# Kernel tuning notes

Measured on AMD Instinct MI355X. Metric: run time of the kernel, lower is better.

## Reference

```python
import jax, jax.numpy as jnp
import numpy as np
import math

B, S, D = 1, 2048, 2048
NH, NKV = 32, 8
HD = D // NH  # 64
N_REP = NH // NKV


def _rope_tables(seq_len, head_dim, base=10000.0):
    half = head_dim // 2
    inv_freq = 1.0 / (base ** (np.arange(half, dtype=np.float32) / half))
    ang = np.arange(seq_len, dtype=np.float32)[:, None] * inv_freq[None, :]  # [S, half]
    ang = np.concatenate([ang, ang], axis=-1)  # [S, head_dim]
    cos = jnp.asarray(np.cos(ang))[:, None, :]  # [S, 1, head_dim]
    sin = jnp.asarray(np.sin(ang))[:, None, :]
    return cos, sin


def setup_inputs() -> dict:
    key = jax.random.key(0)
    ks = jax.random.split(key, 5)
    x = jax.random.normal(ks[0], (B, S, D), dtype=jnp.float32)
    cos, sin = _rope_tables(S, HD)
    # causal additive mask, broadcast over batch/heads
    neg = jnp.float32(-1e9)
    causal = jnp.where(jnp.tril(jnp.ones((S, S), dtype=bool)), 0.0, neg)
    mask = causal[None, None, :, :]  # [1,1,S,S]
    scale = 0.02
    wq = jax.random.normal(ks[1], (D, NH * HD), dtype=jnp.float32) * scale
    wk = jax.random.normal(ks[2], (D, NKV * HD), dtype=jnp.float32) * scale
    wv = jax.random.normal(ks[3], (D, NKV * HD), dtype=jnp.float32) * scale
    wo = jax.random.normal(ks[4], (NH * HD, D), dtype=jnp.float32) * scale
    return {"x": x, "cos": cos, "sin": sin, "mask": mask,
            "wq": wq, "wk": wk, "wv": wv, "wo": wo}


def apply_rotary_emb(x, cos, sin):
    # x: [b, s, h, d]; cos/sin: [s, 1, d] (broadcast over b, h)
    half = x.shape[-1] // 2
    x1, x2 = x[..., :half], x[..., half:]
    c, s = cos[..., :half], sin[..., :half]
    return jnp.concatenate([x1 * c - x2 * s, x1 * s + x2 * c], axis=-1)


def reference(x, cos, sin, mask, wq, wk, wv, wo):
    b, s, _ = x.shape
    q = (x @ wq).reshape(b, s, NH, HD)
    k = (x @ wk).reshape(b, s, NKV, HD)
    v = (x @ wv).reshape(b, s, NKV, HD)
    q = apply_rotary_emb(q, cos, sin)
    k = apply_rotary_emb(k, cos, sin)
    new_k, new_v = k, v  # kv cache (no previous cache)
    # GQA: repeat_interleave kv heads to match query heads
    k_rep = jnp.repeat(k, N_REP, axis=2)  # [b, s, NH, HD]
    v_rep = jnp.repeat(v, N_REP, axis=2)
    scores = jnp.einsum('bqhd,bkhd->bhqk', q, k_rep) / math.sqrt(HD)
    scores = scores + mask[:, :, -s:, :]
    attn = jax.nn.softmax(scores.astype(jnp.float32), axis=-1).astype(q.dtype)
    out = jnp.einsum('bhqk,bkhd->bqhd', attn, v_rep).reshape(b, s, NH * HD)
    return out @ wo, new_k, new_v
```

## Files before the change

### kernel.cpp

```cpp
#include <hip/hip_runtime.h>

#define S_LEN 2048
#define NHQ 32
#define NKV 8
#define HD 64
#define DMODEL 2048
#define DKV 512

typedef unsigned short ushort_t;
typedef unsigned int uint_t;

typedef __attribute__((ext_vector_type(8))) short bf16x8;
typedef __attribute__((ext_vector_type(4))) float f32x4;

__device__ __forceinline__ float b2f(ushort_t h) {
  union { uint_t u; float f; } v;
  v.u = ((uint_t)h) << 16;
  return v.f;
}
__device__ __forceinline__ ushort_t f2b(float f) {
  union { float f; uint_t u; } v;
  v.f = f;
  uint_t r = v.u + 0x7fffu + ((v.u >> 16) & 1u);
  return (ushort_t)(r >> 16);
}
__device__ __forceinline__ uint_t cvt_pk_bf16(float lo, float hi) {
  uint_t r;
  asm("v_cvt_pk_bf16_f32 %0, %1, %2" : "=v"(r) : "v"(lo), "v"(hi));
  return r;
}

union BF8 { uint4 v; ushort_t s[8]; };

__device__ __forceinline__ void gl_lds16(const ushort_t* g, ushort_t* l) {
  __builtin_amdgcn_global_load_lds((const __attribute__((address_space(1))) void*)g,
                                   (__attribute__((address_space(3))) void*)l, 16, 0, 0);
}

__device__ __forceinline__ void wT_tile(const float* __restrict__ W,
                                        ushort_t* __restrict__ WT,
                                        int K, int N, int r0, int c0,
                                        ushort_t (*T)[66], int tid) {
  {
    const int rl = tid >> 2, cp = (tid & 3) * 16;
    const float* p = W + (size_t)(r0 + rl) * N + c0 + cp;
    float v[16];
    *(float4*)(v)      = *(const float4*)(p);
    *(float4*)(v + 4)  = *(const float4*)(p + 4);
    *(float4*)(v + 8)  = *(const float4*)(p + 8);
    *(float4*)(v + 12) = *(const float4*)(p + 12);
    #pragma unroll
    for (int j = 0; j < 16; ++j) T[cp + j][rl] = f2b(v[j]);
  }
  __syncthreads();
  {
    const int cl = tid >> 2, rp = (tid & 3) * 16;
    uint_t u[8];
    #pragma unroll
    for (int i = 0; i < 8; ++i) u[i] = *(const uint_t*)&T[cl][rp + 2 * i];
    ushort_t* outp = WT + (size_t)(c0 + cl) * K + r0 + rp;
    *(uint4*)(outp)     = make_uint4(u[0], u[1], u[2], u[3]);
    *(uint4*)(outp + 8) = make_uint4(u[4], u[5], u[6], u[7]);
  }
}

__global__ __launch_bounds__(256) void prework(const float* __restrict__ X,
                                               ushort_t* __restrict__ XB,
                                               const float* __restrict__ Wq,
                                               const float* __restrict__ Wk,
                                               const float* __restrict__ Wv,
                                               ushort_t* __restrict__ WqT,
                                               ushort_t* __restrict__ WkvT) {
  __shared__ ushort_t T[64][66];
  const int tid = threadIdx.x;
  const int bid = blockIdx.x;
  if (bid < 2048) {
    int i = (bid * 256 + tid) * 8;
    float4 a = *(const float4*)(X + i);
    float4 b = *(const float4*)(X + i + 4);
    BF8 u;
    u.s[0] = f2b(a.x); u.s[1] = f2b(a.y); u.s[2] = f2b(a.z); u.s[3] = f2b(a.w);
    u.s[4] = f2b(b.x); u.s[5] = f2b(b.y); u.s[6] = f2b(b.z); u.s[7] = f2b(b.w);
    *(uint4*)(XB + i) = u.v;
    return;
  }
  const float* W; ushort_t* WT; int N; int local;
  if (bid < 3072)      { local = bid - 2048; W = Wq; WT = WqT;  N = DMODEL; }
  else if (bid < 3328) { local = bid - 3072; W = Wk; WT = WkvT; N = DKV; }
  else                 { local = bid - 3328; W = Wv; WT = WkvT + (size_t)DKV * DMODEL; N = DKV; }
  const int r0 = (local & 31) * 64, c0 = (local >> 5) * 64;
  wT_tile(W, WT, DMODEL, N, r0, c0, T, tid);
}

__global__ __launch_bounds__(256) void postproj(const float* __restrict__ Wo,
                                                ushort_t* __restrict__ WoT,
                                                float* Kio, ushort_t* __restrict__ KB,
                                                const float* __restrict__ cosT,
                                                const float* __restrict__ sinT,
                                                const float* __restrict__ V,
                                                ushort_t* __restrict__ VT) {
  __shared__ ushort_t T[64][66];
  const int tid = threadIdx.x;
  const int bid = blockIdx.x;
  if (bid < 1024) {
    const int r0 = (bid & 31) * 64, c0 = (bid >> 5) * 64;
    wT_tile(Wo, WoT, DMODEL, DMODEL, r0, c0, T, tid);
    return;
  }
  if (bid < 3072) {
    int idx = (bid - 1024) * 256 + tid;
    int d = idx & 31;
    int hk = (idx >> 5) & 7;
    int s = idx >> 8;
    float* p = Kio + (size_t)s * DKV + hk * HD + d;
    float x1 = p[0], x2 = p[32];
    float c = cosT[s * 64 + d], sn = sinT[s * 64 + d];
    float n1 = x1 * c - x2 * sn;
    float n2 = x1 * sn + x2 * c;
    p[0] = n1; p[32] = n2;
    ushort_t* kb = KB + (size_t)hk * S_LEN * HD + (size_t)s * HD + d;
    kb[0] = f2b(n1); kb[32] = f2b(n2);
    return;
  }
  {
    const int local = bid - 3072;
    const int s0 = (local & 31) * 64;
    const int hk = local >> 5;
    {
      const int s_l = tid >> 2, dp = (tid & 3) * 16;
      const float* p = V + (size_t)(s0 + s_l) * DKV + hk * HD + dp;
      float v[16];
      *(float4*)(v)      = *(const float4*)(p);
      *(float4*)(v + 4)  = *(const float4*)(p + 4);
      *(float4*)(v + 8)  = *(const float4*)(p + 8);
      *(float4*)(v + 12) = *(const float4*)(p + 12);
      #pragma unroll
      for (int j = 0; j < 16; ++j) T[dp + j][s_l] = f2b(v[j]);
    }
    __syncthreads();
    {
      const int d_l = tid >> 2, sp = (tid & 3) * 16;
      uint_t u[8];
      #pragma unroll
      for (int i = 0; i < 8; ++i) u[i] = *(const uint_t*)&T[d_l][sp + 2 * i];
      ushort_t* outp = VT + (size_t)hk * HD * S_LEN + (size_t)d_l * S_LEN + s0 + sp;
      *(uint4*)(outp)     = make_uint4(u[0], u[1], u[2], u[3]);
      *(uint4*)(outp + 8) = make_uint4(u[4], u[5], u[6], u[7]);
    }
  }
}

__device__ __forceinline__ void gemm_core_db64(const ushort_t* __restrict__ A,
                                               const ushort_t* __restrict__ BT,
                                               int K, int tile_m, int tile_n,
                                               f32x4 (&acc)[4][2],
                                               ushort_t* AsBase,
                                               ushort_t* BsBase) {
  const int tid = threadIdx.x;
  const int lane = tid & 63;
  const int w = tid >> 6;
  const int wr = (w >> 2) * 64, wc = (w & 3) * 32;
  const int lm = lane & 15, kq = lane >> 4;
  const int BUF = 2 * 128 * 32;
  const int HALF = 128 * 32;

  #pragma unroll
  for (int i = 0; i < 4; ++i)
    #pragma unroll
    for (int j = 0; j < 2; ++j) acc[i][j] = {0.f, 0.f, 0.f, 0.f};

  const ushort_t* ap = A  + (size_t)(tile_m + w * 16 + (lane >> 2)) * K + (lane & 3) * 8;
  const ushort_t* bp = BT + (size_t)(tile_n + w * 16 + (lane >> 2)) * K + (lane & 3) * 8;
  ushort_t* asw = AsBase + w * 512;
  ushort_t* bsw = BsBase + w * 512;

  gl_lds16(ap,      asw);
  gl_lds16(ap + 32, asw + HALF);
  gl_lds16(bp,      bsw);
  gl_lds16(bp + 32, bsw + HALF);
  __syncthreads();

  int cur = 0;
  for (int kt = 0; kt < K; kt += 64) {
    if (kt + 64 < K) {
      const int nb = (cur ^ 1) * BUF;
      gl_lds16(ap + kt + 64, asw + nb);
      gl_lds16(ap + kt + 96, asw + nb + HALF);
      gl_lds16(bp + kt + 64, bsw + nb);
      gl_lds16(bp + kt + 96, bsw + nb + HALF);
    }
    const ushort_t* ac = AsBase + cur * BUF;
    const ushort_t* bc = BsBase + cur * BUF;
    #pragma unroll
    for (int kc = 0; kc < 2; ++kc) {
      bf16x8 af[4], bfr[2];
      #pragma unroll
      for (int i = 0; i < 4; ++i)
        af[i]  = *(const bf16x8*)(ac + kc * HALF + (wr + 16 * i + lm) * 32 + kq * 8);
      #pragma unroll
      for (int j = 0; j < 2; ++j)
        bfr[j] = *(const bf16x8*)(bc + kc * HALF + (wc + 16 * j + lm) * 32 + kq * 8);
      #pragma unroll
      for (int i = 0; i < 4; ++i)
        #pragma unroll
        for (int j = 0; j < 2; ++j)
          acc[i][j] = __builtin_amdgcn_mfma_f32_16x16x32_bf16(af[i], bfr[j], acc[i][j], 0, 0, 0);
    }
    __syncthreads();
    cur ^= 1;
  }
}

__global__ __launch_bounds__(512) void gemm_proj(const ushort_t* __restrict__ A,
                                                 const ushort_t* __restrict__ BT,
                                                 ushort_t* __restrict__ Qo,
                                                 float* __restrict__ Ko,
                                                 float* __restrict__ Vo) {
  __shared__ ushort_t As[2][2][128][32];
  __shared__ ushort_t Bs[2][2][128][32];
  const int lane = threadIdx.x & 63;
  const int w = threadIdx.x >> 6;
  const int wr = (w >> 2) * 64, wc = (w & 3) * 32;
  const int lm = lane & 15, kq = lane >> 4;
  const int tile_m = blockIdx.y * 128, tile_n = blockIdx.x * 128;
  f32x4 acc[4][2];
  gemm_core_db64(A, BT, DMODEL, tile_m, tile_n, acc, &As[0][0][0][0], &Bs[0][0][0][0]);
  #pragma unroll
  for (int i = 0; i < 4; ++i)
    #pragma unroll
    for (int j = 0; j < 2; ++j)
      #pragma unroll
      for (int r = 0; r < 4; ++r) {
        const int row = tile_m + wr + 16 * i + kq * 4 + r;
        const int col = tile_n + wc + 16 * j + lm;
        const float v = acc[i][j][r];
        if (col < 2048)      Qo[(size_t)row * DMODEL + col] = f2b(v);
        else if (col < 2560) Ko[(size_t)row * DKV + col - 2048] = v;
        else                 Vo[(size_t)row * DKV + col - 2560] = v;
      }
}

__global__ __launch_bounds__(512) void gemm_out(const ushort_t* __restrict__ A,
                                                const ushort_t* __restrict__ BT,
                                                float* __restrict__ C) {
  __shared__ ushort_t As[2][2][128][32];
  __shared__ ushort_t Bs[2][2][128][32];
  const int lane = threadIdx.x & 63;
  const int w = threadIdx.x >> 6;
  const int wr = (w >> 2) * 64, wc = (w & 3) * 32;
  const int lm = lane & 15, kq = lane >> 4;
  const int tile_m = blockIdx.y * 128, tile_n = blockIdx.x * 128;
  f32x4 acc[4][2];
  gemm_core_db64(A, BT, DMODEL, tile_m, tile_n, acc, &As[0][0][0][0], &Bs[0][0][0][0]);
  #pragma unroll
  for (int i = 0; i < 4; ++i)
    #pragma unroll
    for (int j = 0; j < 2; ++j)
      #pragma unroll
      for (int r = 0; r < 4; ++r) {
        const int row = tile_m + wr + 16 * i + kq * 4 + r;
        const int col = tile_n + wc + 16 * j + lm;
        C[(size_t)row * DMODEL + col] = acc[i][j][r];
      }
}

__global__ __launch_bounds__(256, 4) void attn_mfma7(const ushort_t* Q,
                                                     const ushort_t* __restrict__ KB,
                                                     const ushort_t* __restrict__ VT,
                                                     const float* __restrict__ cosT,
                                                     const float* __restrict__ sinT,
                                                     ushort_t* O) {
  __shared__ __align__(16) char smem[20480];
  ushort_t (*Ps)[32][72] = (ushort_t (*)[32][72])smem;
  const int wv = threadIdx.x >> 6;
  const int lane = threadIdx.x & 63;
  const int lm = lane & 15, kq = lane >> 4;
  const int bid = blockIdx.x;
  const int xcd = bid & 7;
  const int idx = bid >> 3;
  const int h = (xcd << 2) | (idx & 3);
  const int g = 63 - (idx >> 2);
  const int q0 = g * 32;
  const int hk = h >> 2;
  const ushort_t* KBh = KB + (size_t)hk * S_LEN * HD;
  const ushort_t* VTh = VT + (size_t)hk * HD * S_LEN;
  const float SCL = 0.125f * 1.44269504f;

  bf16x8 bq[2][2];
  #pragma unroll
  for (int nt = 0; nt < 2; ++nt) {
    const int row = q0 + 16 * nt + lm;
    const ushort_t* qp = Q + (size_t)row * DMODEL + h * HD + 8 * kq;
    bf16x8 x1v = *(const bf16x8*)qp;
    bf16x8 x2v = *(const bf16x8*)(qp + 32);
    const float* cp = cosT + row * 64 + 8 * kq;
    const float* sp = sinT + row * 64 + 8 * kq;
    float c[8], s[8];
    *(float4*)(c)     = *(const float4*)(cp);
    *(float4*)(c + 4) = *(const float4*)(cp + 4);
    *(float4*)(s)     = *(const float4*)(sp);
    *(float4*)(s + 4) = *(const float4*)(sp + 4);
    BF8 o1, o2;
    #pragma unroll
    for (int j = 0; j < 8; ++j) {
      float x1 = b2f((ushort_t)x1v[j]);
      float x2 = b2f((ushort_t)x2v[j]);
      o1.s[j] = f2b((x1 * c[j] - x2 * s[j]) * SCL);
      o2.s[j] = f2b((x1 * s[j] + x2 * c[j]) * SCL);
    }
    bq[nt][0] = *(const bf16x8*)&o1;
    bq[nt][1] = *(const bf16x8*)&o2;
  }

  f32x4 Oa[4][2];
  #pragma unroll
  for (int mt = 0; mt < 4; ++mt) { Oa[mt][0] = {0.f,0.f,0.f,0.f}; Oa[mt][1] = {0.f,0.f,0.f,0.f}; }
  float m[2] = {-1e30f, -1e30f};
  float l[2] = {0.f, 0.f};

  const int ntiles = (g >> 1) + 1;
  for (int t = wv; t < ntiles; t += 4) {
    const int base = t * 64;
    f32x4 sc[4][2];
    #pragma unroll
    for (int mt = 0; mt < 4; ++mt) { sc[mt][0] = {0.f,0.f,0.f,0.f}; sc[mt][1] = {0.f,0.f,0.f,0.f}; }
    #pragma unroll
    for (int kc = 0; kc < 2; ++kc) {
      bf16x8 ak[4];
      #pragma unroll
      for (int mt = 0; mt < 4; ++mt)
        ak[mt] = *(const bf16x8*)&KBh[(size_t)(base + 16 * mt + lm) * HD + 8 * kq + 32 * kc];
      #pragma unroll
      for (int mt = 0; mt < 4; ++mt)
        #pragma unroll
        for (int nt = 0; nt < 2; ++nt)
          sc[mt][nt] = __builtin_amdgcn_mfma_f32_16x16x32_bf16(ak[mt], bq[nt][kc], sc[mt][nt], 0, 0, 0);
    }
    const bool diag = (t == ntiles - 1);
    #pragma unroll
    for (int nt = 0; nt < 2; ++nt) {
      const int qg = q0 + 16 * nt + lm;
      if (diag) {
        #pragma unroll
        for (int mt = 0; mt < 4; ++mt)
          #pragma unroll
          for (int r = 0; r < 4; ++r)
            if (base + 16 * mt + 4 * kq + r > qg) sc[mt][nt][r] = -1e9f;
      }
      float lmx = sc[0][nt][0];
      #pragma unroll
      for (int mt = 0; mt < 4; ++mt)
        #pragma unroll
        for (int r = 0; r < 4; ++r) lmx = fmaxf(lmx, sc[mt][nt][r]);
      if (!__all(lmx <= m[nt] + 8.f)) {
        float mx = fmaxf(lmx, __shfl_xor(lmx, 16));
        mx = fmaxf(mx, __shfl_xor(mx, 32));
        const float mn = fmaxf(m[nt], mx);
        const float al = exp2f(m[nt] - mn);
        m[nt] = mn;
        l[nt] *= al;
        #pragma unroll
        for (int mt = 0; mt < 4; ++mt)
          #pragma unroll
          for (int r = 0; r < 4; ++r) Oa[mt][nt][r] *= al;
      }
      float sum = 0.f;
      #pragma unroll
      for (int mt = 0; mt < 4; ++mt)
        #pragma unroll
        for (int r = 0; r < 4; ++r) {
          float p = exp2f(sc[mt][nt][r] - m[nt]);
          sc[mt][nt][r] = p;
          sum += p;
        }
      l[nt] += sum;
      ushort_t* pw = &Ps[wv][16 * nt + lm][4 * kq];
      #pragma unroll
      for (int mt = 0; mt < 4; ++mt)
        *(uint2*)(pw + 16 * mt) = make_uint2(cvt_pk_bf16(sc[mt][nt][0], sc[mt][nt][1]),
                                             cvt_pk_bf16(sc[mt][nt][2], sc[mt][nt][3]));
    }
    #pragma unroll
    for (int kc = 0; kc < 2; ++kc) {
      bf16x8 av[4], pb[2];
      #pragma unroll
      for (int mt = 0; mt < 4; ++mt)
        av[mt] = *(const bf16x8*)&VTh[(size_t)(16 * mt + lm) * S_LEN + base + 8 * kq + 32 * kc];
      #pragma unroll
      for (int nt = 0; nt < 2; ++nt)
        pb[nt] = *(const bf16x8*)&Ps[wv][16 * nt + lm][8 * kq + 32 * kc];
      #pragma unroll
      for (int mt = 0; mt < 4; ++mt)
        #pragma unroll
        for (int nt = 0; nt < 2; ++nt)
          Oa[mt][nt] = __builtin_amdgcn_mfma_f32_16x16x32_bf16(av[mt], pb[nt], Oa[mt][nt], 0, 0, 0);
    }
  }
  #pragma unroll
  for (int nt = 0; nt < 2; ++nt) {
    l[nt] += __shfl_xor(l[nt], 16);
    l[nt] += __shfl_xor(l[nt], 32);
  }

  float* CoB = (float*)smem;
  float* CmB = (float*)smem + 2 * 64 * 36;
  float* ClB = CmB + 2 * 2 * 64;
  __syncthreads();
  if (wv & 1) {
    const int slot = wv >> 1;
    float* myo = CoB + (size_t)(slot * 64 + lane) * 36;
    #pragma unroll
    for (int mt = 0; mt < 4; ++mt)
      #pragma unroll
      for (int nt = 0; nt < 2; ++nt)
        *(f32x4*)(myo + (mt * 2 + nt) * 4) = Oa[mt][nt];
    #pragma unroll
    for (int nt = 0; nt < 2; ++nt) {
      CmB[(slot * 2 + nt) * 64 + lane] = m[nt];
      ClB[(slot * 2 + nt) * 64 + lane] = l[nt];
    }
  }
  __syncthreads();
  if (!(wv & 1)) {
    const int slot = wv >> 1;
    const float* po = CoB + (size_t)(slot * 64 + lane) * 36;
    #pragma unroll
    for (int nt = 0; nt < 2; ++nt) {
      const float m1 = CmB[(slot * 2 + nt) * 64 + lane];
      const float l1 = ClB[(slot * 2 + nt) * 64 + lane];
      const float mn = fmaxf(m[nt], m1);
      const float a0 = exp2f(m[nt] - mn);
      const float a1 = exp2f(m1 - mn);
      m[nt] = mn;
      l[nt] = l[nt] * a0 + l1 * a1;
      #pragma unroll
      for (int mt = 0; mt < 4; ++mt) {
        const f32x4 ov = *(const f32x4*)(po + (mt * 2 + nt) * 4);
        #pragma unroll
        for (int r = 0; r < 4; ++r) Oa[mt][nt][r] = Oa[mt][nt][r] * a0 + ov[r] * a1;
      }
    }
  }
  __syncthreads();
  if (wv == 2) {
    float* myo = CoB + (size_t)lane * 36;
    #pragma unroll
    for (int mt = 0; mt < 4; ++mt)
      #pragma unroll
      for (int nt = 0; nt < 2; ++nt)
        *(f32x4*)(myo + (mt * 2 + nt) * 4) = Oa[mt][nt];
    #pragma unroll
    for (int nt = 0; nt < 2; ++nt) {
      CmB[nt * 64 + lane] = m[nt];
      ClB[nt * 64 + lane] = l[nt];
    }
  }
  __syncthreads();
  if (wv == 0) {
    const float* po = CoB + (size_t)lane * 36;
    #pragma unroll
    for (int nt = 0; nt < 2; ++nt) {
      const float m1 = CmB[nt * 64 + lane];
      const float l1 = ClB[nt * 64 + lane];
      const float mn = fmaxf(m[nt], m1);
      const float a0 = exp2f(m[nt] - mn);
      const float a1 = exp2f(m1 - mn);
      const float inv = 1.f / (l[nt] * a0 + l1 * a1);
      ushort_t* orow = O + (size_t)(q0 + 16 * nt + lm) * DMODEL + h * HD + 4 * kq;
      #pragma unroll
      for (int mt = 0; mt < 4; ++mt) {
        const f32x4 ov = *(const f32x4*)(po + (mt * 2 + nt) * 4);
        const float v0 = (Oa[mt][nt][0] * a0 + ov[0] * a1) * inv;
        const float v1 = (Oa[mt][nt][1] * a0 + ov[1] * a1) * inv;
        const float v2 = (Oa[mt][nt][2] * a0 + ov[2] * a1) * inv;
        const float v3 = (Oa[mt][nt][3] * a0 + ov[3] * a1) * inv;
        *(uint2*)(orow + 16 * mt) = make_uint2(cvt_pk_bf16(v0, v1), cvt_pk_bf16(v2, v3));
      }
    }
  }
}

extern "C" void kernel_launch(void* const* d_in, const int* in_sizes, int n_in,
                              void* d_out, int out_size, void* d_ws, size_t ws_size,
                              hipStream_t stream) {
  const float* x    = (const float*)d_in[0];
  const float* cosT = (const float*)d_in[1];
  const float* sinT = (const float*)d_in[2];
  const float* wq   = (const float*)d_in[4];
  const float* wk   = (const float*)d_in[5];
  const float* wv   = (const float*)d_in[6];
  const float* wo   = (const float*)d_in[7];

  float* out   = (float*)d_out;
  float* out_k = out + (size_t)S_LEN * DMODEL;
  float* out_v = out_k + (size_t)S_LEN * DKV;

  const size_t MB = 1024 * 1024;
  ushort_t* ws    = (ushort_t*)d_ws;
  ushort_t* wqT   = ws;
  ushort_t* wkT   = ws + 4 * MB;
  ushort_t* ws_q  = ws + 6 * MB;
  ushort_t* ws_kb = ws + 10 * MB;
  ushort_t* ws_vt = ws + 11 * MB;
  ushort_t* xb    = (ushort_t*)out;

  dim3 blk(256);
  dim3 blk8(512);
  prework<<<3584, blk, 0, stream>>>(x, xb, wq, wk, wv, wqT, wkT);
  gemm_proj<<<dim3(3072 / 128, S_LEN / 128), blk8, 0, stream>>>(xb, wqT, ws_q, out_k, out_v);
  postproj<<<3328, blk, 0, stream>>>(wo, wqT, out_k, ws_kb, cosT, sinT, out_v, ws_vt);
  attn_mfma7<<<NHQ * 64, blk, 0, stream>>>(ws_q, ws_kb, ws_vt, cosT, sinT, ws_q);
  gemm_out<<<dim3(DMODEL / 128, S_LEN / 128), blk8, 0, stream>>>(ws_q, wqT, out);
}
```

Before: 265.7 us.

## Replace GEMM double buffer with 4-stage K=32 LDS pipeline using vmcnt waits

```diff
diff --git a/kernel.cpp b/kernel.cpp
--- a/kernel.cpp
+++ b/kernel.cpp
@@ -150,7 +150,7 @@
   }
 }
 
-__device__ __forceinline__ void gemm_core_db64(const ushort_t* __restrict__ A,
+__device__ __forceinline__ void gemm_core_pipe(const ushort_t* __restrict__ A,
                                                const ushort_t* __restrict__ BT,
                                                int K, int tile_m, int tile_n,
                                                f32x4 (&acc)[4][2],
@@ -161,8 +161,7 @@
   const int w = tid >> 6;
   const int wr = (w >> 2) * 64, wc = (w & 3) * 32;
   const int lm = lane & 15, kq = lane >> 4;
-  const int BUF = 2 * 128 * 32;
-  const int HALF = 128 * 32;
+  const int BUFS = 128 * 32;
 
   #pragma unroll
   for (int i = 0; i < 4; ++i)
@@ -175,39 +174,40 @@
   ushort_t* bsw = BsBase + w * 512;
 
   gl_lds16(ap,      asw);
-  gl_lds16(ap + 32, asw + HALF);
   gl_lds16(bp,      bsw);
-  gl_lds16(bp + 32, bsw + HALF);
-  __syncthreads();
-
-  int cur = 0;
-  for (int kt = 0; kt < K; kt += 64) {
-    if (kt + 64 < K) {
-      const int nb = (cur ^ 1) * BUF;
-      gl_lds16(ap + kt + 64, asw + nb);
-      gl_lds16(ap + kt + 96, asw + nb + HALF);
-      gl_lds16(bp + kt + 64, bsw + nb);
-      gl_lds16(bp + kt + 96, bsw + nb + HALF);
-    }
-    const ushort_t* ac = AsBase + cur * BUF;
-    const ushort_t* bc = BsBase + cur * BUF;
-    #pragma unroll
-    for (int kc = 0; kc < 2; ++kc) {
-      bf16x8 af[4], bfr[2];
-      #pragma unroll
-      for (int i = 0; i < 4; ++i)
-        af[i]  = *(const bf16x8*)(ac + kc * HALF + (wr + 16 * i + lm) * 32 + kq * 8);
+  gl_lds16(ap + 32, asw + BUFS);
+  gl_lds16(bp + 32, bsw + BUFS);
+  asm volatile("s_waitcnt vmcnt(2)" ::: "memory");
+  __builtin_amdgcn_s_barrier();
+  __builtin_amdgcn_sched_barrier(0);
+
+  const int NT = K / 32;
+  for (int t = 0; t < NT; ++t) {
+    const int cb = t & 3;
+    const bool pf = (t + 2 < NT);
+    if (pf) {
+      const int nb = (t + 2) & 3;
+      gl_lds16(ap + (t + 2) * 32, asw + nb * BUFS);
+      gl_lds16(bp + (t + 2) * 32, bsw + nb * BUFS);
+    }
+    const ushort_t* ac = AsBase + cb * BUFS;
+    const ushort_t* bc = BsBase + cb * BUFS;
+    bf16x8 af[4], bfr[2];
+    #pragma unroll
+    for (int i = 0; i < 4; ++i)
+      af[i]  = *(const bf16x8*)(ac + (wr + 16 * i + lm) * 32 + kq * 8);
+    #pragma unroll
+    for (int j = 0; j < 2; ++j)
+      bfr[j] = *(const bf16x8*)(bc + (wc + 16 * j + lm) * 32 + kq * 8);
+    #pragma unroll
+    for (int i = 0; i < 4; ++i)
       #pragma unroll
       for (int j = 0; j < 2; ++j)
-        bfr[j] = *(const bf16x8*)(bc + kc * HALF + (wc + 16 * j + lm) * 32 + kq * 8);
-      #pragma unroll
-      for (int i = 0; i < 4; ++i)
-        #pragma unroll
-        for (int j = 0; j < 2; ++j)
-          acc[i][j] = __builtin_amdgcn_mfma_f32_16x16x32_bf16(af[i], bfr[j], acc[i][j], 0, 0, 0);
-    }
-    __syncthreads();
-    cur ^= 1;
+        acc[i][j] = __builtin_amdgcn_mfma_f32_16x16x32_bf16(af[i], bfr[j], acc[i][j], 0, 0, 0);
+    if (pf) asm volatile("s_waitcnt vmcnt(2)" ::: "memory");
+    else    asm volatile("s_waitcnt vmcnt(0)" ::: "memory");
+    __builtin_amdgcn_s_barrier();
+    __builtin_amdgcn_sched_barrier(0);
   }
 }
 
@@ -216,15 +216,15 @@
                                                  ushort_t* __restrict__ Qo,
                                                  float* __restrict__ Ko,
                                                  float* __restrict__ Vo) {
-  __shared__ ushort_t As[2][2][128][32];
-  __shared__ ushort_t Bs[2][2][128][32];
+  __shared__ ushort_t As[4][128][32];
+  __shared__ ushort_t Bs[4][128][32];
   const int lane = threadIdx.x & 63;
   const int w = threadIdx.x >> 6;
   const int wr = (w >> 2) * 64, wc = (w & 3) * 32;
   const int lm = lane & 15, kq = lane >> 4;
   const int tile_m = blockIdx.y * 128, tile_n = blockIdx.x * 128;
   f32x4 acc[4][2];
-  gemm_core_db64(A, BT, DMODEL, tile_m, tile_n, acc, &As[0][0][0][0], &Bs[0][0][0][0]);
+  gemm_core_pipe(A, BT, DMODEL, tile_m, tile_n, acc, &As[0][0][0], &Bs[0][0][0]);
   #pragma unroll
   for (int i = 0; i < 4; ++i)
     #pragma unroll
@@ -243,15 +243,15 @@
 __global__ __launch_bounds__(512) void gemm_out(const ushort_t* __restrict__ A,
                                                 const ushort_t* __restrict__ BT,
                                                 float* __restrict__ C) {
-  __shared__ ushort_t As[2][2][128][32];
-  __shared__ ushort_t Bs[2][2][128][32];
+  __shared__ ushort_t As[4][128][32];
+  __shared__ ushort_t Bs[4][128][32];
   const int lane = threadIdx.x & 63;
   const int w = threadIdx.x >> 6;
   const int wr = (w >> 2) * 64, wc = (w & 3) * 32;
   const int lm = lane & 15, kq = lane >> 4;
   const int tile_m = blockIdx.y * 128, tile_n = blockIdx.x * 128;
   f32x4 acc[4][2];
-  gemm_core_db64(A, BT, DMODEL, tile_m, tile_n, acc, &As[0][0][0][0], &Bs[0][0][0][0]);
+  gemm_core_pipe(A, BT, DMODEL, tile_m, tile_n, acc, &As[0][0][0], &Bs[0][0][0]);
   #pragma unroll
   for (int i = 0; i < 4; ++i)
     #pragma unroll
```

Measured after the change: 287.9 us. +8.4%, slower.
